# Performance work log

Hardware: AMD Instinct MI355X
Metric: run time of the kernel (lower is better)

## Reference

```python
import jax, jax.numpy as jnp
import numpy as np

H, D = 16, 64            # total_num_heads, head_dim
E = H * D                # embed_dim = 1024
NUM_BUCKETS, MAX_DIST = 32, 128
SCALING = D ** -0.5


def _rel_buckets(seq_len):
    # WavLM bidirectional relative position buckets (static, computed in numpy)
    ctx = np.arange(seq_len)[:, None]
    mem = np.arange(seq_len)[None, :]
    rel = mem - ctx                                  # [s, s]
    nb = NUM_BUCKETS // 2
    buckets = (rel > 0).astype(np.int64) * nb
    rp = np.abs(rel)
    max_exact = nb // 2
    is_small = rp < max_exact
    large = max_exact + (
        np.log(np.maximum(rp, 1) / max_exact) / np.log(MAX_DIST / max_exact) * (nb - max_exact)
    ).astype(np.int64)
    large = np.minimum(large, nb - 1)
    buckets = buckets + np.where(is_small, rp, large)
    return jnp.asarray(buckets)


def setup_inputs() -> dict:
    key = jax.random.key(0)
    ks = jax.random.split(key, 12)
    s = 0.02
    x = jax.random.normal(ks[0], (8, 1024, E), jnp.float32)
    Wq = jax.random.normal(ks[1], (E, H * D), jnp.float32) * s
    bq = jnp.zeros((H * D,), jnp.float32)
    Wk = jax.random.normal(ks[2], (E, H * D), jnp.float32) * s
    bk = jnp.zeros((H * D,), jnp.float32)
    Wv = jax.random.normal(ks[3], (E, H * D), jnp.float32) * s
    bv = jnp.zeros((H * D,), jnp.float32)
    Wo = jax.random.normal(ks[4], (H * D, E), jnp.float32) * s
    bo = jnp.zeros((E,), jnp.float32)
    rel_embed = jax.random.normal(ks[5], (NUM_BUCKETS, H), jnp.float32) * s
    gru_w = jax.random.normal(ks[6], (D, 8), jnp.float32) * s
    gru_b = jnp.zeros((8,), jnp.float32)
    gru_const = jnp.ones((1, H, 1, 1), jnp.float32)
    return {"x": x, "Wq": Wq, "bq": bq, "Wk": Wk, "bk": bk, "Wv": Wv, "bv": bv,
            "Wo": Wo, "bo": bo, "rel_embed": rel_embed,
            "gru_w": gru_w, "gru_b": gru_b, "gru_const": gru_const}


def reference(x, Wq, bq, Wk, bk, Wv, bv, Wo, bo, rel_embed, gru_w, gru_b, gru_const):
    b, s, e = x.shape
    # relative position bias: [H, s, s]
    buckets = _rel_buckets(s)
    pos_bias = jnp.transpose(rel_embed[buckets], (2, 0, 1))
    # gated relative position (gru_rel_pos)
    qlayer = x.reshape(b, s, H, D).transpose(0, 2, 1, 3)            # [b,H,s,D]
    g = jnp.einsum('bhsd,de->bhse', qlayer, gru_w) + gru_b          # [b,H,s,8]
    g = jax.nn.sigmoid(g.reshape(b, H, s, 2, 4).sum(-1))           # [b,H,s,2]
    gate_a, gate_b = g[..., :1], g[..., 1:]                         # [b,H,s,1]
    gate = gate_a * (gate_b * gru_const - 1.0) + 2.0                # [b,H,s,1]
    bias = gate * pos_bias[None]                                    # [b,H,s,s]
    # projections -> [b,H,s,D]
    q = (x @ Wq + bq).reshape(b, s, H, D).transpose(0, 2, 1, 3)
    k = (x @ Wk + bk).reshape(b, s, H, D).transpose(0, 2, 1, 3)
    v = (x @ Wv + bv).reshape(b, s, H, D).transpose(0, 2, 1, 3)
    scores = SCALING * jnp.einsum('bhqd,bhkd->bhqk', q, k) + bias
    w = jax.nn.softmax(scores, axis=-1)   # includes stable max-subtract
    out = jnp.einsum('bhqk,bhkd->bhqd', w, v)
    out = out.transpose(0, 2, 1, 3).reshape(b, s, H * D)
    return out @ Wo + bo
```

## Files before the change

### kernel.cpp

```cpp
#include <hip/hip_runtime.h>
#include <hip/hip_bf16.h>
#include <math.h>


typedef __attribute__((ext_vector_type(8))) short short8;
typedef __attribute__((ext_vector_type(4))) float f32x4;

#define LDSP(p) ((__attribute__((address_space(3))) void*)(p))
#define GLBP(p) ((const __attribute__((address_space(1))) void*)(p))

__device__ __forceinline__ void async_ld16(const void* src, void* dst) {
  __builtin_amdgcn_global_load_lds(GLBP(src), LDSP(dst), 16, 0, 0);
}
__device__ __forceinline__ unsigned short f2bf(float f) {
  __hip_bfloat16 h = __float2bfloat16(f);
  return __builtin_bit_cast(unsigned short, h);
}
#if __has_builtin(__builtin_amdgcn_exp2f)
#define EXP2(x) __builtin_amdgcn_exp2f(x)
#else
#define EXP2(x) exp2f(x)
#endif

__global__ __launch_bounds__(256) void prep_all(
    const float* __restrict__ x, const float* __restrict__ gw,
    const float* __restrict__ gb, const float* __restrict__ gcst,
    const float* __restrict__ W0, const float* __restrict__ W1,
    const float* __restrict__ W2, const float* __restrict__ W3,
    const float* __restrict__ rel_embed,
    unsigned short* __restrict__ xb, float* __restrict__ gate_ws,
    unsigned short* __restrict__ Wt_all, float* __restrict__ btab) {
  __shared__ __align__(16) float tile[64][68];
  const int bid = blockIdx.x, t = threadIdx.x;
  if (bid < 8192) {
    float* xr = &tile[0][0];
    const float4 v = *(const float4*)&x[(size_t)bid * 1024 + t * 4];
    *(float4*)&xr[t * 4] = v;
    ushort4 o;
    o.x = f2bf(v.x); o.y = f2bf(v.y); o.z = f2bf(v.z); o.w = f2bf(v.w);
    *(ushort4*)&xb[(size_t)bid * 1024 + t * 4] = o;
    __syncthreads();
    const int h = t >> 4, i = t & 15;
    float pa = 0.f, pb = 0.f;
    #pragma unroll
    for (int j = 0; j < 4; ++j) {
      const int d = i * 4 + j;
      const float xv = xr[h * 64 + d];
      const float* wr = &gw[d * 8];
      pa += xv * (wr[0] + wr[1] + wr[2] + wr[3]);
      pb += xv * (wr[4] + wr[5] + wr[6] + wr[7]);
    }
    #pragma unroll
    for (int msk = 1; msk <= 8; msk <<= 1) {
      pa += __shfl_xor(pa, msk);
      pb += __shfl_xor(pb, msk);
    }
    if (i == 0) {
      const float ba = gb[0] + gb[1] + gb[2] + gb[3];
      const float bb = gb[4] + gb[5] + gb[6] + gb[7];
      const float ga  = 1.f / (1.f + __expf(-(pa + ba)));
      const float gbv = 1.f / (1.f + __expf(-(pb + bb)));
      const float gv  = ga * (gbv * gcst[h] - 1.f) + 2.f;
      const int b = bid >> 10, s = bid & 1023;
      gate_ws[(b * 16 + h) * 1024 + s] = gv;
    }
  } else if (bid < 9216) {
    const int zz = bid - 8192;
    const int z = zz >> 8;
    const float* W = (z == 0) ? W0 : (z == 1) ? W1 : (z == 2) ? W2 : W3;
    unsigned short* Wt = Wt_all + (size_t)z * 1048576;
    const int n0 = (zz & 15) * 64, k0 = ((zz >> 4) & 15) * 64;
    const int c = (t & 15) * 4, r = t >> 4;
    #pragma unroll
    for (int i = 0; i < 4; ++i)
      *(float4*)&tile[r + i * 16][c] =
          *(const float4*)&W[(size_t)(k0 + r + i * 16) * 1024 + n0 + c];
    __syncthreads();
    #pragma unroll
    for (int i = 0; i < 4; ++i) {
      const int n = r + i * 16;
      ushort4 o;
      o.x = f2bf(tile[c + 0][n]); o.y = f2bf(tile[c + 1][n]);
      o.z = f2bf(tile[c + 2][n]); o.w = f2bf(tile[c + 3][n]);
      *(ushort4*)&Wt[(size_t)(n0 + n) * 1024 + k0 + c] = o;
    }
  } else {
    const int idx = (bid - 9216) * 256 + t;
    if (idx < 2047) {
      const int rel = idx - 1023;
      int bucket = (rel > 0) ? 16 : 0;
      const int rp = rel < 0 ? -rel : rel;
      if (rp < 8) {
        bucket += rp;
      } else {
        const double lv = log((double)rp / 8.0) / log(16.0) * 8.0;
        int large = 8 + (int)lv;
        bucket += (large < 15) ? large : 15;
      }
      #pragma unroll
      for (int h = 0; h < 16; ++h)
        btab[h * 2048 + idx] = rel_embed[bucket * 16 + h];
    }
  }
}

template <int SWAP>
__device__ __forceinline__ void gemm_core(
    const unsigned short* __restrict__ A, const unsigned short* __restrict__ Bt,
    unsigned short* As, unsigned short* Bs, const int m0, const int n0,
    f32x4 acc[4][4]) {
  const int t = threadIdx.x, w = t >> 6, l = t & 63;
  const int lr = l & 15, lg = l >> 4;
  const int wr = w >> 1, wc = w & 1;

  const unsigned short* asrc[4];
  const unsigned short* bsrc[4];
  unsigned short* adst[4];
  unsigned short* bdst[4];
  #pragma unroll
  for (int i = 0; i < 4; ++i) {
    const int p = (w * 4 + i) * 64 + l, r = p >> 3, c = p & 7;
    const int cs = c ^ (r & 7);
    asrc[i] = A + (size_t)(m0 + r) * 1024 + cs * 8;
    bsrc[i] = Bt + (size_t)(n0 + r) * 1024 + cs * 8;
    adst[i] = &As[(w * 4 + i) * 512];
    bdst[i] = &Bs[(w * 4 + i) * 512];
  }

  int offA[2][4], offB[2][4];
  #pragma unroll
  for (int ks = 0; ks < 2; ++ks)
    #pragma unroll
    for (int mt = 0; mt < 4; ++mt) {
      offA[ks][mt] = (wr * 64 + mt * 16 + lr) * 64 + ((ks * 4 + lg) ^ (lr & 7)) * 8;
      offB[ks][mt] = (wc * 64 + mt * 16 + lr) * 64 + ((ks * 4 + lg) ^ (lr & 7)) * 8;
    }

  for (int k0 = 0; k0 < 16; ++k0) {
    #pragma unroll
    for (int i = 0; i < 4; ++i) {
      async_ld16(asrc[i], adst[i]);
      async_ld16(bsrc[i], bdst[i]);
      asrc[i] += 64;
      bsrc[i] += 64;
    }
    __syncthreads();
    #pragma unroll
    for (int ks = 0; ks < 2; ++ks) {
      short8 af[4], bf[4];
      #pragma unroll
      for (int mt = 0; mt < 4; ++mt) af[mt] = *(const short8*)&As[offA[ks][mt]];
      #pragma unroll
      for (int nt = 0; nt < 4; ++nt) bf[nt] = *(const short8*)&Bs[offB[ks][nt]];
      #pragma unroll
      for (int mt = 0; mt < 4; ++mt)
        #pragma unroll
        for (int nt = 0; nt < 4; ++nt)
          acc[mt][nt] = SWAP
              ? __builtin_amdgcn_mfma_f32_16x16x32_bf16(bf[nt], af[mt], acc[mt][nt], 0, 0, 0)
              : __builtin_amdgcn_mfma_f32_16x16x32_bf16(af[mt], bf[nt], acc[mt][nt], 0, 0, 0);
    }
    __syncthreads();
  }
}

__global__ __launch_bounds__(256) void gemm_qkv(
    const unsigned short* __restrict__ A, const unsigned short* __restrict__ wt_all,
    const float* __restrict__ bq, const float* __restrict__ bk,
    const float* __restrict__ bv, unsigned short* __restrict__ q_ws,
    unsigned short* __restrict__ k_ws, unsigned short* __restrict__ vt_ws) {
  __shared__ __align__(16) unsigned short As[128 * 64];
  __shared__ __align__(16) unsigned short Bs[128 * 64];
  const int which = blockIdx.y >> 3;
  const int m0 = blockIdx.x * 128, n0 = (blockIdx.y & 7) * 128;
  const unsigned short* Bt = wt_all + (size_t)which * 1048576;

  const int t = threadIdx.x, w = t >> 6, l = t & 63;
  const int lr = l & 15, lg = l >> 4;
  const int wr = w >> 1, wc = w & 1;
  const int mbase = m0 + wr * 64, nbase = n0 + wc * 64;

  f32x4 acc[4][4];
  #pragma unroll
  for (int mt = 0; mt < 4; ++mt)
    #pragma unroll
    for (int nt = 0; nt < 4; ++nt) acc[mt][nt] = (f32x4){0.f, 0.f, 0.f, 0.f};

  if (which == 2) {
    gemm_core<0>(A, Bt, As, Bs, m0, n0, acc);
    #pragma unroll
    for (int mt = 0; mt < 4; ++mt) {
      const int m4 = mbase + mt * 16 + lg * 4;
      const int b = m4 >> 10, s = m4 & 1023;
      #pragma unroll
      for (int nt = 0; nt < 4; ++nt) {
        const int n = nbase + nt * 16 + lr, h = n >> 6, d = n & 63;
        const float bvv = bv[n];
        ushort4 o;
        o.x = f2bf(acc[mt][nt][0] + bvv);
        o.y = f2bf(acc[mt][nt][1] + bvv);
        o.z = f2bf(acc[mt][nt][2] + bvv);
        o.w = f2bf(acc[mt][nt][3] + bvv);
        *(ushort4*)&vt_ws[(size_t)(b * 16 + h) * 65536 + (size_t)d * 1024 + s] = o;
      }
    }
  } else {
    gemm_core<1>(A, Bt, As, Bs, m0, n0, acc);
    unsigned short* dst = (which == 0) ? q_ws : k_ws;
    const float* bias = (which == 0) ? bq : bk;
    const float scale = (which == 0) ? 0.18033688011f : 1.0f;
    #pragma unroll
    for (int nt = 0; nt < 4; ++nt) {
      const int n4 = nbase + nt * 16 + lg * 4;
      const int h = n4 >> 6, d = n4 & 63;
      const float4 b4 = *(const float4*)&bias[n4];
      #pragma unroll
      for (int mt = 0; mt < 4; ++mt) {
        const int m = mbase + mt * 16 + lr;
        const int b = m >> 10, s = m & 1023;
        ushort4 o;
        o.x = f2bf((acc[mt][nt][0] + b4.x) * scale);
        o.y = f2bf((acc[mt][nt][1] + b4.y) * scale);
        o.z = f2bf((acc[mt][nt][2] + b4.z) * scale);
        o.w = f2bf((acc[mt][nt][3] + b4.w) * scale);
        *(ushort4*)&dst[(size_t)(b * 16 + h) * 65536 + s * 64 + d] = o;
      }
    }
  }
}

__global__ __launch_bounds__(256) void gemm_out(
    const unsigned short* __restrict__ A, const unsigned short* __restrict__ Bt,
    const float* __restrict__ bias, float* __restrict__ C) {
  __shared__ __align__(16) unsigned short As[128 * 64];
  __shared__ __align__(16) unsigned short Bs[128 * 64];
  const int m0 = blockIdx.x * 128, n0 = blockIdx.y * 128;
  f32x4 acc[4][4];
  #pragma unroll
  for (int mt = 0; mt < 4; ++mt)
    #pragma unroll
    for (int nt = 0; nt < 4; ++nt) acc[mt][nt] = (f32x4){0.f, 0.f, 0.f, 0.f};
  gemm_core<1>(A, Bt, As, Bs, m0, n0, acc);

  const int t = threadIdx.x, w = t >> 6, l = t & 63;
  const int lr = l & 15, lg = l >> 4;
  const int wr = w >> 1, wc = w & 1;
  const int mbase = m0 + wr * 64, nbase = n0 + wc * 64;
  #pragma unroll
  for (int nt = 0; nt < 4; ++nt) {
    const int n4 = nbase + nt * 16 + lg * 4;
    const float4 b4 = *(const float4*)&bias[n4];
    #pragma unroll
    for (int mt = 0; mt < 4; ++mt) {
      const int m = mbase + mt * 16 + lr;
      float4 o;
      o.x = acc[mt][nt][0] + b4.x;
      o.y = acc[mt][nt][1] + b4.y;
      o.z = acc[mt][nt][2] + b4.z;
      o.w = acc[mt][nt][3] + b4.w;
      *(float4*)&C[(size_t)m * 1024 + n4] = o;
    }
  }
}

__global__ __launch_bounds__(256) void attn_mfma(
    const unsigned short* __restrict__ q_ws, const unsigned short* __restrict__ k_ws,
    const unsigned short* __restrict__ vt_ws, const float* __restrict__ gate_ws,
    const float* __restrict__ btab, unsigned short* __restrict__ ctx) {
  __shared__ __align__(16) unsigned short Ks[2][64 * 64];
  __shared__ __align__(16) unsigned short Vts[64 * 64];
  __shared__ __align__(16) unsigned short Ps[4 * 1024];
  __shared__ __align__(16) float biasl[1088];
  __shared__ float gates[64];
  __shared__ float scl[64];

  const int t = threadIdx.x, w = t >> 6, l = t & 63;
  const int lr = l & 15, lg = l >> 4;
  const int bh = blockIdx.x, h = bh & 15, b = bh >> 4;
  const int q0 = blockIdx.y * 64;
  const size_t hb = (size_t)bh * 65536;

  short8 qf[2];
  #pragma unroll
  for (int ks = 0; ks < 2; ++ks)
    qf[ks] = *(const short8*)(q_ws + hb + (size_t)(q0 + w * 16 + lr) * 64 +
                              (ks * 4 + lg) * 8);

  #pragma unroll
  for (int i = 0; i < 2; ++i) {
    const int p = (w * 2 + i) * 64 + l, r = p >> 3, c = p & 7;
    const int cs = c ^ (r & 7);
    async_ld16(k_ws + hb + (size_t)r * 64 + cs * 8, &Ks[0][(w * 2 + i) * 512]);
  }
  {
    const float* bt = btab + h * 2048 + (960 - q0);
    for (int u = t * 4; u < 1088; u += 1024)
      *(float4*)&biasl[u] = *(const float4*)&bt[u];
  }
  if (t < 64) gates[t] = gate_ws[bh * 1024 + q0 + t];
  asm volatile("s_waitcnt vmcnt(0) lgkmcnt(0)" ::: "memory");
  __builtin_amdgcn_s_barrier();
  __builtin_amdgcn_sched_barrier(0);

  int pwoff[4], proff[2], offF[2][4];
  #pragma unroll
  for (int nt = 0; nt < 4; ++nt)
    pwoff[nt] = w * 2048 + ((lr * 128 + nt * 32 + lg * 8) ^ ((lr & 7) << 4));
  #pragma unroll
  for (int ks = 0; ks < 2; ++ks) {
    proff[ks] = w * 2048 + ((lr * 128 + ks * 64 + lg * 16) ^ ((lr & 7) << 4));
    #pragma unroll
    for (int nt = 0; nt < 4; ++nt)
      offF[ks][nt] = (nt * 16 + lr) * 64 + ((ks * 4 + lg) ^ (lr & 7)) * 8;
  }

  float mcur = -1e30f, lsum = 0.f;
  f32x4 acc_o[4];
  #pragma unroll
  for (int dt = 0; dt < 4; ++dt) acc_o[dt] = (f32x4){0.f, 0.f, 0.f, 0.f};
  const float gtl = gates[w * 16 + lr] * 1.44269504f;
  const int ub = 63 - w * 16 - lr;
  char* Pb = (char*)Ps;

  int pcur = 0;
  for (int kt = 0; kt < 16; ++kt) {
    #pragma unroll
    for (int i = 0; i < 2; ++i) {
      const int p = (w * 2 + i) * 64 + l, r = p >> 3, c = p & 7;
      const int cs = c ^ (r & 7);
      async_ld16(vt_ws + hb + (size_t)r * 1024 + kt * 64 + cs * 8,
                 &Vts[(w * 2 + i) * 512]);
    }
    if (kt < 15) {
      #pragma unroll
      for (int i = 0; i < 2; ++i) {
        const int p = (w * 2 + i) * 64 + l, r = p >> 3, c = p & 7;
        const int cs = c ^ (r & 7);
        async_ld16(k_ws + hb + (size_t)(kt + 1) * 4096 + (size_t)r * 64 + cs * 8,
                   &Ks[pcur ^ 1][(w * 2 + i) * 512]);
      }
    }

    f32x4 accs[4];
    #pragma unroll
    for (int nt = 0; nt < 4; ++nt) accs[nt] = (f32x4){0.f, 0.f, 0.f, 0.f};
    __builtin_amdgcn_s_setprio(1);
    #pragma unroll
    for (int ks = 0; ks < 2; ++ks) {
      #pragma unroll
      for (int nt = 0; nt < 4; ++nt) {
        const short8 kf = *(const short8*)&Ks[pcur][offF[ks][nt]];
        accs[nt] = __builtin_amdgcn_mfma_f32_16x16x32_bf16(kf, qf[ks], accs[nt], 0, 0, 0);
      }
    }
    __builtin_amdgcn_s_setprio(0);

    const int bb = kt * 64 + ub + lg * 4;
    float tm = -1e30f;
    #pragma unroll
    for (int nt = 0; nt < 4; ++nt) {
      #pragma unroll
      for (int i = 0; i < 4; ++i) {
        const float sv = accs[nt][i] + gtl * biasl[bb + nt * 16 + i];
        accs[nt][i] = sv;
      }
      tm = fmaxf(fmaxf(tm, fmaxf(accs[nt][0], accs[nt][1])),
                 fmaxf(accs[nt][2], accs[nt][3]));
    }
    tm = fmaxf(tm, __shfl_xor(tm, 16));
    tm = fmaxf(tm, __shfl_xor(tm, 32));

    const int skip = __all(tm <= mcur + 11.5f);
    float sc = 1.0f;
    if (!skip) {
      const float mn = fmaxf(mcur, tm);
      sc = EXP2(mcur - mn);
      mcur = mn;
      if (lg == 0) scl[w * 16 + lr] = sc;
    }

    float ps = 0.f;
    #pragma unroll
    for (int nt = 0; nt < 4; ++nt) {
      const float p0 = EXP2(accs[nt][0] - mcur);
      const float p1 = EXP2(accs[nt][1] - mcur);
      const float p2 = EXP2(accs[nt][2] - mcur);
      const float p3 = EXP2(accs[nt][3] - mcur);
      ps += (p0 + p1) + (p2 + p3);
      short4 pk;
      pk.x = (short)f2bf(p0); pk.y = (short)f2bf(p1);
      pk.z = (short)f2bf(p2); pk.w = (short)f2bf(p3);
      *(short4*)(Pb + pwoff[nt]) = pk;
    }
    ps += __shfl_xor(ps, 16);
    ps += __shfl_xor(ps, 32);
    lsum = skip ? (lsum + ps) : (lsum * sc + ps);

    if (kt < 15) {
      asm volatile("s_waitcnt vmcnt(2) lgkmcnt(0)" ::: "memory");
    } else {
      asm volatile("s_waitcnt vmcnt(0) lgkmcnt(0)" ::: "memory");
    }
    __builtin_amdgcn_s_barrier();
    __builtin_amdgcn_sched_barrier(0);

    if (!skip) {
      const float s0 = scl[w * 16 + lg * 4 + 0];
      const float s1 = scl[w * 16 + lg * 4 + 1];
      const float s2 = scl[w * 16 + lg * 4 + 2];
      const float s3 = scl[w * 16 + lg * 4 + 3];
      #pragma unroll
      for (int dt = 0; dt < 4; ++dt) {
        acc_o[dt][0] *= s0; acc_o[dt][1] *= s1;
        acc_o[dt][2] *= s2; acc_o[dt][3] *= s3;
      }
    }

    __builtin_amdgcn_s_setprio(1);
    #pragma unroll
    for (int ks = 0; ks < 2; ++ks) {
      const short8 pf = *(const short8*)(Pb + proff[ks]);
      #pragma unroll
      for (int dt = 0; dt < 4; ++dt) {
        const short8 vf = *(const short8*)&Vts[offF[ks][dt]];
        acc_o[dt] = __builtin_amdgcn_mfma_f32_16x16x32_bf16(pf, vf, acc_o[dt], 0, 0, 0);
      }
    }
    __builtin_amdgcn_s_setprio(0);

    asm volatile("s_waitcnt vmcnt(0)" ::: "memory");
    __builtin_amdgcn_s_barrier();
    __builtin_amdgcn_sched_barrier(0);
    pcur ^= 1;
  }

  if (lg == 0) scl[w * 16 + lr] = 1.0f / lsum;
  asm volatile("s_waitcnt lgkmcnt(0)" ::: "memory");
  __builtin_amdgcn_sched_barrier(0);
  float inv[4];
  #pragma unroll
  for (int i = 0; i < 4; ++i) inv[i] = scl[w * 16 + lg * 4 + i];
  #pragma unroll
  for (int i = 0; i < 4; ++i) {
    const int q = q0 + w * 16 + lg * 4 + i;
    const size_t rowoff = ((size_t)(b * 1024 + q) * 16 + h) * 64;
    #pragma unroll
    for (int dt = 0; dt < 4; ++dt)
      ctx[rowoff + dt * 16 + lr] = f2bf(acc_o[dt][i] * inv[i]);
  }
}

extern "C" void kernel_launch(void* const* d_in, const int* in_sizes, int n_in,
                              void* d_out, int out_size, void* d_ws, size_t ws_size,
                              hipStream_t stream) {
  const float* x    = (const float*)d_in[0];
  const float* Wq   = (const float*)d_in[1];
  const float* bq   = (const float*)d_in[2];
  const float* Wk   = (const float*)d_in[3];
  const float* bk   = (const float*)d_in[4];
  const float* Wv   = (const float*)d_in[5];
  const float* bv   = (const float*)d_in[6];
  const float* Wo   = (const float*)d_in[7];
  const float* bo   = (const float*)d_in[8];
  const float* rel  = (const float*)d_in[9];
  const float* gw   = (const float*)d_in[10];
  const float* gb   = (const float*)d_in[11];
  const float* gcst = (const float*)d_in[12];
  float* out = (float*)d_out;

  char* ws = (char*)d_ws;
  unsigned short* x_bf   = (unsigned short*)(ws);
  unsigned short* wt_all = (unsigned short*)(ws + 16777216);
  unsigned short* q_ws   = (unsigned short*)(ws + 25165824);
  unsigned short* k_ws   = (unsigned short*)(ws + 41943040);
  unsigned short* vt_ws  = (unsigned short*)(ws + 58720256);
  unsigned short* ctx    = (unsigned short*)(ws + 75497472);
  float* gate = (float*)(ws + 92274688);
  float* btab = (float*)(ws + 92798976);

  prep_all <<<dim3(9224),    256, 0, stream>>>(x, gw, gb, gcst, Wq, Wk, Wv, Wo,
                                               rel, x_bf, gate, wt_all, btab);
  gemm_qkv <<<dim3(64, 24),  256, 0, stream>>>(x_bf, wt_all, bq, bk, bv,
                                               q_ws, k_ws, vt_ws);
  attn_mfma<<<dim3(128, 16), 256, 0, stream>>>(q_ws, k_ws, vt_ws, gate, btab, ctx);
  gemm_out <<<dim3(64, 8),   256, 0, stream>>>(ctx, wt_all + 3 * 1048576, bo, out);
}
```

Measured before the change: 292.0 us.

## Double attention query tile to 128 rows with 8 waves per block

The attention kernel now runs 512 threads (8 waves) per block, each block covering 128 query rows, so every K/V tile staged in LDS is shared by twice as many waves. Each thread issues one async load per tile instead of two. The relative-position bias is preloaded into the score accumulator before the QK MFMA instead of being added afterwards. The per-row sum shuffle reduction moves out of the key loop to the end. This halves K/V global traffic and per-block load instructions, at the cost of fewer blocks (1024), more LDS per block, and a 512-thread barrier domain.

Result: faster. 286.2 us (-2.0%).

```diff
diff --git a/kernel.cpp b/kernel.cpp
--- a/kernel.cpp
+++ b/kernel.cpp
@@ -263,21 +263,21 @@
   }
 }
 
-__global__ __launch_bounds__(256) void attn_mfma(
+__global__ __launch_bounds__(512) void attn_mfma(
     const unsigned short* __restrict__ q_ws, const unsigned short* __restrict__ k_ws,
     const unsigned short* __restrict__ vt_ws, const float* __restrict__ gate_ws,
     const float* __restrict__ btab, unsigned short* __restrict__ ctx) {
   __shared__ __align__(16) unsigned short Ks[2][64 * 64];
   __shared__ __align__(16) unsigned short Vts[64 * 64];
-  __shared__ __align__(16) unsigned short Ps[4 * 1024];
-  __shared__ __align__(16) float biasl[1088];
-  __shared__ float gates[64];
-  __shared__ float scl[64];
+  __shared__ __align__(16) unsigned short Ps[8 * 1024];
+  __shared__ __align__(16) float biasl[1216];
+  __shared__ float gates[128];
+  __shared__ float scl[128];
 
   const int t = threadIdx.x, w = t >> 6, l = t & 63;
   const int lr = l & 15, lg = l >> 4;
   const int bh = blockIdx.x, h = bh & 15, b = bh >> 4;
-  const int q0 = blockIdx.y * 64;
+  const int q0 = blockIdx.y * 128;
   const size_t hb = (size_t)bh * 65536;
 
   short8 qf[2];
@@ -286,18 +286,17 @@
     qf[ks] = *(const short8*)(q_ws + hb + (size_t)(q0 + w * 16 + lr) * 64 +
                               (ks * 4 + lg) * 8);
 
-  #pragma unroll
-  for (int i = 0; i < 2; ++i) {
-    const int p = (w * 2 + i) * 64 + l, r = p >> 3, c = p & 7;
+  {
+    const int p = t, r = p >> 3, c = p & 7;
     const int cs = c ^ (r & 7);
-    async_ld16(k_ws + hb + (size_t)r * 64 + cs * 8, &Ks[0][(w * 2 + i) * 512]);
+    async_ld16(k_ws + hb + (size_t)r * 64 + cs * 8, &Ks[0][w * 512]);
   }
   {
-    const float* bt = btab + h * 2048 + (960 - q0);
-    for (int u = t * 4; u < 1088; u += 1024)
-      *(float4*)&biasl[u] = *(const float4*)&bt[u];
-  }
-  if (t < 64) gates[t] = gate_ws[bh * 1024 + q0 + t];
+    const float* bt = btab + h * 2048 + (896 - q0);
+    const int u = t * 4;
+    if (u < 1216) *(float4*)&biasl[u] = *(const float4*)&bt[u];
+  }
+  if (t < 128) gates[t] = gate_ws[bh * 1024 + q0 + t];
   asm volatile("s_waitcnt vmcnt(0) lgkmcnt(0)" ::: "memory");
   __builtin_amdgcn_s_barrier();
   __builtin_amdgcn_sched_barrier(0);
@@ -319,31 +318,30 @@
   #pragma unroll
   for (int dt = 0; dt < 4; ++dt) acc_o[dt] = (f32x4){0.f, 0.f, 0.f, 0.f};
   const float gtl = gates[w * 16 + lr] * 1.44269504f;
-  const int ub = 63 - w * 16 - lr;
+  const int ub = 127 - w * 16 - lr;
   char* Pb = (char*)Ps;
 
   int pcur = 0;
   for (int kt = 0; kt < 16; ++kt) {
-    #pragma unroll
-    for (int i = 0; i < 2; ++i) {
-      const int p = (w * 2 + i) * 64 + l, r = p >> 3, c = p & 7;
+    {
+      const int p = t, r = p >> 3, c = p & 7;
       const int cs = c ^ (r & 7);
-      async_ld16(vt_ws + hb + (size_t)r * 1024 + kt * 64 + cs * 8,
-                 &Vts[(w * 2 + i) * 512]);
-    }
-    if (kt < 15) {
-      #pragma unroll
-      for (int i = 0; i < 2; ++i) {
-        const int p = (w * 2 + i) * 64 + l, r = p >> 3, c = p & 7;
-        const int cs = c ^ (r & 7);
+      async_ld16(vt_ws + hb + (size_t)r * 1024 + kt * 64 + cs * 8, &Vts[w * 512]);
+      if (kt < 15)
         async_ld16(k_ws + hb + (size_t)(kt + 1) * 4096 + (size_t)r * 64 + cs * 8,
-                   &Ks[pcur ^ 1][(w * 2 + i) * 512]);
-      }
-    }
-
+                   &Ks[pcur ^ 1][w * 512]);
+    }
+
+    const int bb = kt * 64 + ub + lg * 4;
     f32x4 accs[4];
     #pragma unroll
-    for (int nt = 0; nt < 4; ++nt) accs[nt] = (f32x4){0.f, 0.f, 0.f, 0.f};
+    for (int nt = 0; nt < 4; ++nt) {
+      accs[nt][0] = gtl * biasl[bb + nt * 16 + 0];
+      accs[nt][1] = gtl * biasl[bb + nt * 16 + 1];
+      accs[nt][2] = gtl * biasl[bb + nt * 16 + 2];
+      accs[nt][3] = gtl * biasl[bb + nt * 16 + 3];
+    }
+
     __builtin_amdgcn_s_setprio(1);
     #pragma unroll
     for (int ks = 0; ks < 2; ++ks) {
@@ -355,18 +353,11 @@
     }
     __builtin_amdgcn_s_setprio(0);
 
-    const int bb = kt * 64 + ub + lg * 4;
     float tm = -1e30f;
     #pragma unroll
-    for (int nt = 0; nt < 4; ++nt) {
-      #pragma unroll
-      for (int i = 0; i < 4; ++i) {
-        const float sv = accs[nt][i] + gtl * biasl[bb + nt * 16 + i];
-        accs[nt][i] = sv;
-      }
+    for (int nt = 0; nt < 4; ++nt)
       tm = fmaxf(fmaxf(tm, fmaxf(accs[nt][0], accs[nt][1])),
                  fmaxf(accs[nt][2], accs[nt][3]));
-    }
     tm = fmaxf(tm, __shfl_xor(tm, 16));
     tm = fmaxf(tm, __shfl_xor(tm, 32));
 
@@ -392,12 +383,10 @@
       pk.z = (short)f2bf(p2); pk.w = (short)f2bf(p3);
       *(short4*)(Pb + pwoff[nt]) = pk;
     }
-    ps += __shfl_xor(ps, 16);
-    ps += __shfl_xor(ps, 32);
     lsum = skip ? (lsum + ps) : (lsum * sc + ps);
 
     if (kt < 15) {
-      asm volatile("s_waitcnt vmcnt(2) lgkmcnt(0)" ::: "memory");
+      asm volatile("s_waitcnt vmcnt(1) lgkmcnt(0)" ::: "memory");
     } else {
       asm volatile("s_waitcnt vmcnt(0) lgkmcnt(0)" ::: "memory");
     }
@@ -434,9 +423,11 @@
     pcur ^= 1;
   }
 
+  lsum += __shfl_xor(lsum, 16);
+  lsum += __shfl_xor(lsum, 32);
   if (lg == 0) scl[w * 16 + lr] = 1.0f / lsum;
   asm volatile("s_waitcnt lgkmcnt(0)" ::: "memory");
-  __builtin_amdgcn_sched_barrier(0);
+  __builtin_amdgcn_s_barrier();
   float inv[4];
   #pragma unroll
   for (int i = 0; i < 4; ++i) inv[i] = scl[w * 16 + lg * 4 + i];
@@ -478,10 +469,10 @@
   float* gate = (float*)(ws + 92274688);
   float* btab = (float*)(ws + 92798976);
 
-  prep_all <<<dim3(9224),    256, 0, stream>>>(x, gw, gb, gcst, Wq, Wk, Wv, Wo,
-                                               rel, x_bf, gate, wt_all, btab);
-  gemm_qkv <<<dim3(64, 24),  256, 0, stream>>>(x_bf, wt_all, bq, bk, bv,
-                                               q_ws, k_ws, vt_ws);
-  attn_mfma<<<dim3(128, 16), 256, 0, stream>>>(q_ws, k_ws, vt_ws, gate, btab, ctx);
-  gemm_out <<<dim3(64, 8),   256, 0, stream>>>(ctx, wt_all + 3 * 1048576, bo, out);
-}
+  prep_all <<<dim3(9224),   256, 0, stream>>>(x, gw, gb, gcst, Wq, Wk, Wv, Wo,
+                                              rel, x_bf, gate, wt_all, btab);
+  gemm_qkv <<<dim3(64, 24), 256, 0, stream>>>(x_bf, wt_all, bq, bk, bv,
+                                              q_ws, k_ws, vt_ws);
+  attn_mfma<<<dim3(128, 8), 512, 0, stream>>>(q_ws, k_ws, vt_ws, gate, btab, ctx);
+  gemm_out <<<dim3(64, 8),  256, 0, stream>>>(ctx, wt_all + 3 * 1048576, bo, out);
+}
```
